# Performance work log

Measured on AMD Instinct MI355X. Metric: run time of the kernel, lower is better.

Reference implementation:

```python
import jax, jax.numpy as jnp
import numpy as np

N, B, D, S, STDDEV = 129, 128, 64, 2, 0.5  # N odd so the site before the last is an input site
NOUT = int(np.ceil((N - 1) / S) + 1)  # 65
NIN = N - NOUT                        # 64


def setup_inputs() -> dict:
    key = jax.random.key(0)
    k1, k2, k3 = jax.random.split(key, 3)
    x = jax.random.normal(k1, (N, B, 2), jnp.float32)
    mps_input = STDDEV * jax.random.normal(k2, (NIN, D, D, 2), jnp.float32)
    mps_output = STDDEV * jax.random.normal(k3, (NOUT, D, D, 2, 2), jnp.float32)
    return {"x": x, "mps_input": mps_input, "mps_output": mps_output}


def _forward(x, mps_input, mps_output):
    # ---- batched MPS contraction (call) ----
    # S=2: even sites are output sites, odd sites are input sites.
    X = jnp.einsum('nbi,nlrij->nblrj', x[::2], mps_output)      # (Nout,B,D,D,2)
    A_in = jnp.einsum('nbi,nlri->nblr', x[1::2], mps_input)     # (Nin,B,D,D)
    # middle mps blocks: A_in[k-1] contracted with X[k] for k=1..Nout-2
    mps_mid = jnp.einsum('nblr,nbrdi->nbldi', A_in[:-1], X[1:-1])   # (Nout-2,B,D,D,2)
    mps_last = jnp.einsum('blr,brdi->bldi', A_in[-1], X[-1][:, :, :1])  # (B,D,1,2)
    A0 = X[0][:, 0]  # first block restricted to l=0 -> (B,D,2)

    Al = jnp.einsum('bui,bdi->bud', A0, A0)  # (B,D,D), PSD

    def step(Al, A):
        amax = jnp.max(jnp.abs(Al), axis=(1, 2), keepdims=True)
        Aln = Al / amax
        T = jnp.einsum('bdu,bdli->blui', Aln, A)
        return jnp.einsum('blui,buri->blr', T, A), jnp.log(amax[:, 0, 0])

    Al, logs = jax.lax.scan(step, Al, mps_mid)   # logs: (Nout-2, B)
    Al, last_log = step(Al, mps_last)            # Al: (B,1,1)
    out = jnp.sum(logs, axis=0) + last_log + jnp.log(Al[:, 0, 0])  # (B,)

    # ---- log_norm: scalar DxD transfer-matrix chain ----
    Al0 = jnp.zeros((D, D), x.dtype).at[0, 0].set(1.0)

    def contract_out(M2, Mo):
        T = jnp.einsum('du,dkij->kuij', M2, Mo)
        return jnp.einsum('kuij,ulij->kl', T, Mo)

    def contract_in(M2, Mi):
        T = jnp.einsum('du,dki->kui', M2, Mi)
        return jnp.einsum('kui,uli->kl', T, Mi)

    # site 0: amax of initial Al is exactly 1 (log 0), then contract output tensor 0
    Aln = contract_out(Al0, mps_output[0])

    def nstep(M2, Ms):
        Mi, Mo = Ms
        a1 = jnp.max(jnp.abs(M2)); M2 = contract_in(M2 / a1, Mi)
        a2 = jnp.max(jnp.abs(M2)); M2 = contract_out(M2 / a2, Mo)
        return M2, jnp.log(a1) + jnp.log(a2)

    AlN, nlogs = jax.lax.scan(nstep, Aln, (mps_input, mps_output[1:]))
    lnrm = jnp.sum(nlogs) + jnp.log(AlN[0, 0])
    return out, lnrm


def reference(x, mps_input, mps_output):
    return _forward(x, mps_input, mps_output)
```

## Files before the change

### kernel.cpp

```cpp
#include <hip/hip_runtime.h>
#include <math.h>

#define TPB 512
#define LDM 72
#define SLOTS 4608


typedef __attribute__((ext_vector_type(8))) short bf16x8;
typedef __attribute__((ext_vector_type(4))) float f32x4;
typedef unsigned short US;

__device__ __forceinline__ US f2b(float f) {
    union { float f; unsigned u; } v; v.f = f;
    return (US)((v.u + 0x7FFFu + ((v.u >> 16) & 1u)) >> 16);
}
__device__ __forceinline__ float bf2f(US h) {
    union { unsigned u; float f; } v; v.u = ((unsigned)h) << 16; return v.f;
}

struct Frag { bf16x8 lo, hi; };

__device__ __forceinline__ Frag ldf(const US* buf, int row0, int lane) {
    const US* p = buf + (row0 + (lane & 15)) * LDM + ((lane >> 4) << 3);
    Frag f; f.lo = *(const bf16x8*)p; f.hi = *(const bf16x8*)(p + 32); return f;
}
__device__ __forceinline__ f32x4 mm(const Frag& a, const Frag& b, f32x4 c) {
    c = __builtin_amdgcn_mfma_f32_16x16x32_bf16(a.lo, b.lo, c, 0, 0, 0);
    c = __builtin_amdgcn_mfma_f32_16x16x32_bf16(a.hi, b.hi, c, 0, 0, 0);
    return c;
}
__device__ __forceinline__ void stt(US* dst, f32x4 d, float s,
                                    int col0, int row0, int lane) {
    ushort4 wv;
    wv.x = f2b(d.x * s); wv.y = f2b(d.y * s);
    wv.z = f2b(d.z * s); wv.w = f2b(d.w * s);
    *(ushort4*)(dst + (col0 + (lane & 15)) * LDM + row0 + ((lane >> 4) << 2)) = wv;
}

template<int NG>
__device__ __forceinline__ void congr16(US* sm, int sSlot, int gSlot, US* Uw,
                                        f32x4 acc[4], int C0, int lane) {
    const US* S = sm + sSlot * SLOTS;
    Frag aS[4];
#pragma unroll
    for (int rt = 0; rt < 4; ++rt) aS[rt] = ldf(S, rt * 16, lane);
#pragma unroll
    for (int g = 0; g < NG; ++g) {
        const US* G = sm + (gSlot + g) * SLOTS;
        US* Ug = Uw + g * (16 * LDM);
        Frag b = ldf(G, C0, lane);
#pragma unroll
        for (int rt = 0; rt < 4; ++rt) {
            f32x4 z = {0.f, 0.f, 0.f, 0.f};
            z = mm(aS[rt], b, z);
            stt(Ug, z, 1.f, 0, rt * 16, lane);
        }
    }
#pragma unroll
    for (int rt = 0; rt < 4; ++rt) acc[rt] = (f32x4){0.f, 0.f, 0.f, 0.f};
#pragma unroll
    for (int g = 0; g < NG; ++g) {
        const US* G = sm + (gSlot + g) * SLOTS;
        const US* Ug = Uw + g * (16 * LDM);
        Frag u = ldf(Ug, 0, lane);
#pragma unroll
        for (int rt = 0; rt < 4; ++rt) {
            Frag ga = ldf(G, rt * 16, lane);
            acc[rt] = mm(ga, u, acc[rt]);
        }
    }
}

__device__ __forceinline__ void stacc16(US* Sb, const f32x4 acc[4], float s,
                                        int C0, int lane) {
#pragma unroll
    for (int rt = 0; rt < 4; ++rt) stt(Sb, acc[rt], s, C0, rt * 16, lane);
}

__device__ __forceinline__ float stmax16(US* Sb, const f32x4 acc[4], float s,
                                         int C0, int lane) {
    float m = 0.f;
#pragma unroll
    for (int rt = 0; rt < 4; ++rt) {
        float vx = acc[rt].x * s, vy = acc[rt].y * s;
        float vz = acc[rt].z * s, vw = acc[rt].w * s;
        m = fmaxf(m, fmaxf(fmaxf(fabsf(vx), fabsf(vy)),
                           fmaxf(fabsf(vz), fabsf(vw))));
        ushort4 wv; wv.x = f2b(vx); wv.y = f2b(vy); wv.z = f2b(vz); wv.w = f2b(vw);
        *(ushort4*)(Sb + (C0 + (lane & 15)) * LDM + rt * 16 + ((lane >> 4) << 2)) = wv;
    }
#pragma unroll
    for (int off = 32; off; off >>= 1) m = fmaxf(m, __shfl_down(m, off, 64));
    return m;
}

__global__ __launch_bounds__(TPB)
void mps_proj_kernel(const float* __restrict__ x,
                     const float* __restrict__ mi,
                     const float* __restrict__ mo,
                     float* __restrict__ out) {
    __shared__ __align__(16) US smem[12 * SLOTS];
#define SL(i) (smem + (i) * SLOTS)
    __shared__ float fsA[256];
    __shared__ float fsp[8];
    __shared__ float fsrA[2][4];
    __shared__ float fsrB[2][4];
    __shared__ float fsv[128];

    const int tid  = threadIdx.x;
    const int lane = tid & 63;
    const int w    = tid >> 6;
    const int C0   = (w & 3) * 16;
    US* const Uw   = smem + (8 + (w & 3)) * SLOTS;

    const float2* mi2 = (const float2*)mi;
    const float4* mo4 = (const float4*)mo;

    float logsum = 0.f;
    f32x4 acc[4];

    if (blockIdx.x < 128) {
        const int b = blockIdx.x;
        const float xa = x[b * 2 + 0], xb = x[b * 2 + 1];
        if (tid < 64) {
            float4 v = mo4[tid];
            fsA[tid * 2 + 0] = xa * v.x + xb * v.z;
            fsA[tid * 2 + 1] = xa * v.y + xb * v.w;
        }
        __syncthreads();
        float vals[8]; float mloc = 0.f;
#pragma unroll
        for (int j = 0; j < 8; ++j) {
            int pos = tid + j * TPB; int u = pos >> 6, d = pos & 63;
            float s = fsA[u * 2] * fsA[d * 2] + fsA[u * 2 + 1] * fsA[d * 2 + 1];
            vals[j] = s; mloc = fmaxf(mloc, fabsf(s));
        }
#pragma unroll
        for (int off = 32; off; off >>= 1) mloc = fmaxf(mloc, __shfl_down(mloc, off, 64));
        if (lane == 0) fsp[w] = mloc;
        __syncthreads();
        float amax = fsp[0];
#pragma unroll
        for (int i = 1; i < 8; ++i) amax = fmaxf(amax, fsp[i]);
        logsum = logf(amax);
        {
            float inv = 1.f / amax;
#pragma unroll
            for (int j = 0; j < 8; ++j) {
                int pos = tid + j * TPB;
                SL(0)[(pos >> 6) * LDM + (pos & 63)] = f2b(vals[j] * inv);
            }
        }
        if (w >= 4) {
            const int j = w - 4;
            const float x1a = x[256 + b * 2 + 0], x1b = x[256 + b * 2 + 1];
            bf16x8 g0, g1;
#pragma unroll
            for (int t = 0; t < 8; ++t) {
                float2 m0 = mi2[(16 * j + t) * 64 + lane];
                float2 m1 = mi2[(16 * j + 8 + t) * 64 + lane];
                g0[t] = (short)f2b(x1a * m0.x + x1b * m0.y);
                g1[t] = (short)f2b(x1a * m1.x + x1b * m1.y);
            }
            *(bf16x8*)(SL(2) + lane * LDM + 16 * j) = g0;
            *(bf16x8*)(SL(2) + lane * LDM + 16 * j + 8) = g1;
        }
        if (tid < 4) fsrB[1][tid] = 1.f;
        __syncthreads();

        for (int k = 0; k < 63; ++k) {
            if (w < 4) {
                congr16<1>(smem, 0, 2, Uw, acc, C0, lane);
                stacc16(SL(1), acc, 1.f, C0, lane);
            } else {
                const int j = w - 4;
                const float x0a = x[(2 * k + 2) * 256 + b * 2 + 0];
                const float x0b = x[(2 * k + 2) * 256 + b * 2 + 1];
                const float4* so = mo4 + (k + 1) * 4096;
                bf16x8 a0, a1, c0, c1;
#pragma unroll
                for (int t = 0; t < 8; ++t) {
                    float4 m0 = so[(16 * j + t) * 64 + lane];
                    float4 m1 = so[(16 * j + 8 + t) * 64 + lane];
                    a0[t] = (short)f2b(x0a * m0.x + x0b * m0.z);
                    c0[t] = (short)f2b(x0a * m0.y + x0b * m0.w);
                    a1[t] = (short)f2b(x0a * m1.x + x0b * m1.z);
                    c1[t] = (short)f2b(x0a * m1.y + x0b * m1.w);
                }
                *(bf16x8*)(SL(4) + lane * LDM + 16 * j) = a0;
                *(bf16x8*)(SL(4) + lane * LDM + 16 * j + 8) = a1;
                *(bf16x8*)(SL(5) + lane * LDM + 16 * j) = c0;
                *(bf16x8*)(SL(5) + lane * LDM + 16 * j + 8) = c1;
            }
            __syncthreads();
            if (w < 4) {
                float a = fmaxf(fmaxf(fsrB[(k + 1) & 1][0], fsrB[(k + 1) & 1][1]),
                                fmaxf(fsrB[(k + 1) & 1][2], fsrB[(k + 1) & 1][3]));
                logsum += logf(a);
                congr16<2>(smem, 1, 4, Uw, acc, C0, lane);
                float m = stmax16(SL(0), acc, 1.f / a, C0, lane);
                if (lane == 0) fsrB[k & 1][w] = m;
            } else {
                const int j = w - 4;
                const float x1a = x[(2 * k + 3) * 256 + b * 2 + 0];
                const float x1b = x[(2 * k + 3) * 256 + b * 2 + 1];
                const float2* si = mi2 + (k + 1) * 4096;
                bf16x8 g0, g1;
#pragma unroll
                for (int t = 0; t < 8; ++t) {
                    float2 m0 = si[(16 * j + t) * 64 + lane];
                    float2 m1 = si[(16 * j + 8 + t) * 64 + lane];
                    g0[t] = (short)f2b(x1a * m0.x + x1b * m0.y);
                    g1[t] = (short)f2b(x1a * m1.x + x1b * m1.y);
                }
                *(bf16x8*)(SL(2) + lane * LDM + 16 * j) = g0;
                *(bf16x8*)(SL(2) + lane * LDM + 16 * j + 8) = g1;
            }
            __syncthreads();
        }

        {
            const float x0a = x[128 * 256 + b * 2 + 0];
            const float x0b = x[128 * 256 + b * 2 + 1];
            if (tid < 64) {
                float4 v = mo4[64 * 4096 + tid * 64];
                fsA[tid * 2 + 0] = x0a * v.x + x0b * v.z;
                fsA[tid * 2 + 1] = x0a * v.y + x0b * v.w;
            }
            __syncthreads();
            if (tid < 128) {
                int dd = tid >> 1, ii = tid & 1;
                float s = 0.f;
                for (int r = 0; r < 64; ++r)
                    s += bf2f(SL(2)[r * LDM + dd]) * fsA[r * 2 + ii];
                fsv[tid] = s;
            }
            __syncthreads();
            float part = 0.f;
#pragma unroll
            for (int j = 0; j < 8; ++j) {
                int pos = tid + j * TPB; int dd = pos >> 6, uu = pos & 63;
                part += bf2f(SL(0)[dd * LDM + uu]) *
                        (fsv[dd * 2] * fsv[uu * 2] + fsv[dd * 2 + 1] * fsv[uu * 2 + 1]);
            }
#pragma unroll
            for (int off = 32; off; off >>= 1) part += __shfl_down(part, off, 64);
            if (lane == 0) fsp[w] = part;
            __syncthreads();
            if (tid == 0) {
                float t = 0.f;
#pragma unroll
                for (int i = 0; i < 8; ++i) t += fsp[i];
                out[b] = logsum + logf(t);
            }
        }
    } else {
        if (tid < 64) {
            float4 v = mo4[tid];
            fsA[tid * 4 + 0] = v.x; fsA[tid * 4 + 1] = v.y;
            fsA[tid * 4 + 2] = v.z; fsA[tid * 4 + 3] = v.w;
        }
        __syncthreads();
        float vals[8]; float mloc = 0.f;
#pragma unroll
        for (int j = 0; j < 8; ++j) {
            int pos = tid + j * TPB; int kk = pos >> 6, ll = pos & 63;
            float s = fsA[kk*4+0]*fsA[ll*4+0] + fsA[kk*4+1]*fsA[ll*4+1] +
                      fsA[kk*4+2]*fsA[ll*4+2] + fsA[kk*4+3]*fsA[ll*4+3];
            vals[j] = s; mloc = fmaxf(mloc, fabsf(s));
        }
#pragma unroll
        for (int off = 32; off; off >>= 1) mloc = fmaxf(mloc, __shfl_down(mloc, off, 64));
        if (lane == 0) fsp[w] = mloc;
        __syncthreads();
        float amax = fsp[0];
#pragma unroll
        for (int i = 1; i < 8; ++i) amax = fmaxf(amax, fsp[i]);
        logsum = logf(amax);
        {
            float inv = 1.f / amax;
#pragma unroll
            for (int j = 0; j < 8; ++j) {
                int pos = tid + j * TPB;
                SL(0)[(pos >> 6) * LDM + (pos & 63)] = f2b(vals[j] * inv);
            }
        }
        if (w >= 4) {
            const int j = w - 4;
            bf16x8 g00, g01, g10, g11;
#pragma unroll
            for (int t = 0; t < 8; ++t) {
                float2 m0 = mi2[(16 * j + t) * 64 + lane];
                float2 m1 = mi2[(16 * j + 8 + t) * 64 + lane];
                g00[t] = (short)f2b(m0.x); g10[t] = (short)f2b(m0.y);
                g01[t] = (short)f2b(m1.x); g11[t] = (short)f2b(m1.y);
            }
            *(bf16x8*)(SL(2) + lane * LDM + 16 * j) = g00;
            *(bf16x8*)(SL(2) + lane * LDM + 16 * j + 8) = g01;
            *(bf16x8*)(SL(3) + lane * LDM + 16 * j) = g10;
            *(bf16x8*)(SL(3) + lane * LDM + 16 * j + 8) = g11;
        }
        if (tid < 4) fsrB[1][tid] = 1.f;
        __syncthreads();

        for (int n = 0; n < 64; ++n) {
            if (w < 4) {
                float aB = fmaxf(fmaxf(fsrB[(n + 1) & 1][0], fsrB[(n + 1) & 1][1]),
                                 fmaxf(fsrB[(n + 1) & 1][2], fsrB[(n + 1) & 1][3]));
                logsum += logf(aB);
                congr16<2>(smem, 0, 2, Uw, acc, C0, lane);
                float m = stmax16(SL(1), acc, 1.f / aB, C0, lane);
                if (lane == 0) fsrA[n & 1][w] = m;
            } else {
                const int j = w - 4;
                const float4* so = mo4 + (n + 1) * 4096;
                bf16x8 g[4][2];
#pragma unroll
                for (int t = 0; t < 8; ++t) {
                    float4 m0 = so[(16 * j + t) * 64 + lane];
                    float4 m1 = so[(16 * j + 8 + t) * 64 + lane];
                    g[0][0][t] = (short)f2b(m0.x); g[1][0][t] = (short)f2b(m0.y);
                    g[2][0][t] = (short)f2b(m0.z); g[3][0][t] = (short)f2b(m0.w);
                    g[0][1][t] = (short)f2b(m1.x); g[1][1][t] = (short)f2b(m1.y);
                    g[2][1][t] = (short)f2b(m1.z); g[3][1][t] = (short)f2b(m1.w);
                }
#pragma unroll
                for (int c = 0; c < 4; ++c) {
                    *(bf16x8*)(SL(4 + c) + lane * LDM + 16 * j) = g[c][0];
                    *(bf16x8*)(SL(4 + c) + lane * LDM + 16 * j + 8) = g[c][1];
                }
            }
            __syncthreads();
            if (w < 4) {
                float aA = fmaxf(fmaxf(fsrA[n & 1][0], fsrA[n & 1][1]),
                                 fmaxf(fsrA[n & 1][2], fsrA[n & 1][3]));
                logsum += logf(aA);
                congr16<4>(smem, 1, 4, Uw, acc, C0, lane);
                float m = stmax16(SL(0), acc, 1.f / aA, C0, lane);
                if (lane == 0) fsrB[n & 1][w] = m;
            } else if (n < 63) {
                const int j = w - 4;
                const float2* si = mi2 + (n + 1) * 4096;
                bf16x8 g00, g01, g10, g11;
#pragma unroll
                for (int t = 0; t < 8; ++t) {
                    float2 m0 = si[(16 * j + t) * 64 + lane];
                    float2 m1 = si[(16 * j + 8 + t) * 64 + lane];
                    g00[t] = (short)f2b(m0.x); g10[t] = (short)f2b(m0.y);
                    g01[t] = (short)f2b(m1.x); g11[t] = (short)f2b(m1.y);
                }
                *(bf16x8*)(SL(2) + lane * LDM + 16 * j) = g00;
                *(bf16x8*)(SL(2) + lane * LDM + 16 * j + 8) = g01;
                *(bf16x8*)(SL(3) + lane * LDM + 16 * j) = g10;
                *(bf16x8*)(SL(3) + lane * LDM + 16 * j + 8) = g11;
            }
            __syncthreads();
        }
        if (tid == 0) out[128] = logsum + logf(bf2f(SL(0)[0]));
    }
#undef SL
}

extern "C" void kernel_launch(void* const* d_in, const int* in_sizes, int n_in,
                              void* d_out, int out_size, void* d_ws, size_t ws_size,
                              hipStream_t stream) {
    (void)in_sizes; (void)n_in; (void)d_ws; (void)ws_size; (void)out_size;
    const float* x  = (const float*)d_in[0];
    const float* mi = (const float*)d_in[1];
    const float* mo = (const float*)d_in[2];
    float* out = (float*)d_out;
    hipLaunchKernelGGL(mps_proj_kernel, dim3(129), dim3(TPB), 0, stream,
                       x, mi, mo, out);
}
```

Measured before the change: 262.6 us.

## Compute full 64x64 congruence in one wave with double-buffered loader waves

The chain contraction moves from four compute waves, each owning a 16-column strip and syncing twice per step with shared-memory amax exchange, to a single wave that computes the whole 64x64 product per half-step and computes the amax in registers. Four loader waves (block shrinks to 320 threads) prefetch both input and output tensors for the next step into double-buffered LDS slots, so there is only one barrier per step. This removes cross-wave reductions and half the barriers, at the cost of serializing four times the MFMA work onto one wave per block.

```diff
diff --git a/kernel.cpp b/kernel.cpp
--- a/kernel.cpp
+++ b/kernel.cpp
@@ -1,7 +1,7 @@
 #include <hip/hip_runtime.h>
 #include <math.h>
 
-#define TPB 512
+#define TPB 320
 #define LDM 72
 #define SLOTS 4608
 
@@ -38,60 +38,62 @@
 }
 
 template<int NG>
-__device__ __forceinline__ void congr16(US* sm, int sSlot, int gSlot, US* Uw,
-                                        f32x4 acc[4], int C0, int lane) {
-    const US* S = sm + sSlot * SLOTS;
+__device__ __forceinline__ void congr_full(US* sm, const US* S, const US* Gb,
+                                           f32x4 acc[4][4], int lane) {
     Frag aS[4];
 #pragma unroll
     for (int rt = 0; rt < 4; ++rt) aS[rt] = ldf(S, rt * 16, lane);
 #pragma unroll
+    for (int rt = 0; rt < 4; ++rt)
+#pragma unroll
+        for (int ct = 0; ct < 4; ++ct) acc[rt][ct] = (f32x4){0.f, 0.f, 0.f, 0.f};
+#pragma unroll
     for (int g = 0; g < NG; ++g) {
-        const US* G = sm + (gSlot + g) * SLOTS;
-        US* Ug = Uw + g * (16 * LDM);
-        Frag b = ldf(G, C0, lane);
-#pragma unroll
-        for (int rt = 0; rt < 4; ++rt) {
-            f32x4 z = {0.f, 0.f, 0.f, 0.f};
-            z = mm(aS[rt], b, z);
-            stt(Ug, z, 1.f, 0, rt * 16, lane);
+        const US* G = Gb + g * SLOTS;
+        US* U = sm + (1 + 13 * (g & 1)) * SLOTS;
+#pragma unroll
+        for (int ct = 0; ct < 4; ++ct) {
+            Frag bG = ldf(G, ct * 16, lane);
+#pragma unroll
+            for (int rt = 0; rt < 4; ++rt) {
+                f32x4 d = {0.f, 0.f, 0.f, 0.f};
+                d = mm(aS[rt], bG, d);
+                stt(U, d, 1.f, ct * 16, rt * 16, lane);
+            }
+        }
+        Frag gA[4];
+#pragma unroll
+        for (int rt = 0; rt < 4; ++rt) gA[rt] = ldf(G, rt * 16, lane);
+#pragma unroll
+        for (int ct = 0; ct < 4; ++ct) {
+            Frag bU = ldf(U, ct * 16, lane);
+#pragma unroll
+            for (int rt = 0; rt < 4; ++rt)
+                acc[rt][ct] = mm(gA[rt], bU, acc[rt][ct]);
         }
     }
-#pragma unroll
-    for (int rt = 0; rt < 4; ++rt) acc[rt] = (f32x4){0.f, 0.f, 0.f, 0.f};
-#pragma unroll
-    for (int g = 0; g < NG; ++g) {
-        const US* G = sm + (gSlot + g) * SLOTS;
-        const US* Ug = Uw + g * (16 * LDM);
-        Frag u = ldf(Ug, 0, lane);
-#pragma unroll
-        for (int rt = 0; rt < 4; ++rt) {
-            Frag ga = ldf(G, rt * 16, lane);
-            acc[rt] = mm(ga, u, acc[rt]);
-        }
-    }
-}
-
-__device__ __forceinline__ void stacc16(US* Sb, const f32x4 acc[4], float s,
-                                        int C0, int lane) {
-#pragma unroll
-    for (int rt = 0; rt < 4; ++rt) stt(Sb, acc[rt], s, C0, rt * 16, lane);
-}
-
-__device__ __forceinline__ float stmax16(US* Sb, const f32x4 acc[4], float s,
-                                         int C0, int lane) {
+}
+
+__device__ __forceinline__ float amax16(const f32x4 acc[4][4]) {
     float m = 0.f;
 #pragma unroll
-    for (int rt = 0; rt < 4; ++rt) {
-        float vx = acc[rt].x * s, vy = acc[rt].y * s;
-        float vz = acc[rt].z * s, vw = acc[rt].w * s;
-        m = fmaxf(m, fmaxf(fmaxf(fabsf(vx), fabsf(vy)),
-                           fmaxf(fabsf(vz), fabsf(vw))));
-        ushort4 wv; wv.x = f2b(vx); wv.y = f2b(vy); wv.z = f2b(vz); wv.w = f2b(vw);
-        *(ushort4*)(Sb + (C0 + (lane & 15)) * LDM + rt * 16 + ((lane >> 4) << 2)) = wv;
-    }
-#pragma unroll
-    for (int off = 32; off; off >>= 1) m = fmaxf(m, __shfl_down(m, off, 64));
+    for (int rt = 0; rt < 4; ++rt)
+#pragma unroll
+        for (int ct = 0; ct < 4; ++ct)
+            m = fmaxf(m, fmaxf(fmaxf(fabsf(acc[rt][ct].x), fabsf(acc[rt][ct].y)),
+                               fmaxf(fabsf(acc[rt][ct].z), fabsf(acc[rt][ct].w))));
+#pragma unroll
+    for (int off = 32; off; off >>= 1) m = fmaxf(m, __shfl_xor(m, off, 64));
     return m;
+}
+
+__device__ __forceinline__ void store16(US* dst, const f32x4 acc[4][4], float s,
+                                        int lane) {
+#pragma unroll
+    for (int rt = 0; rt < 4; ++rt)
+#pragma unroll
+        for (int ct = 0; ct < 4; ++ct)
+            stt(dst, acc[rt][ct], s, ct * 16, rt * 16, lane);
 }
 
 __global__ __launch_bounds__(TPB)
@@ -99,25 +101,21 @@
                      const float* __restrict__ mi,
                      const float* __restrict__ mo,
                      float* __restrict__ out) {
-    __shared__ __align__(16) US smem[12 * SLOTS];
+    __shared__ __align__(16) US smem[15 * SLOTS];
 #define SL(i) (smem + (i) * SLOTS)
     __shared__ float fsA[256];
-    __shared__ float fsp[8];
-    __shared__ float fsrA[2][4];
-    __shared__ float fsrB[2][4];
+    __shared__ float fsr[8];
     __shared__ float fsv[128];
 
     const int tid  = threadIdx.x;
     const int lane = tid & 63;
     const int w    = tid >> 6;
-    const int C0   = (w & 3) * 16;
-    US* const Uw   = smem + (8 + (w & 3)) * SLOTS;
 
     const float2* mi2 = (const float2*)mi;
     const float4* mo4 = (const float4*)mo;
 
     float logsum = 0.f;
-    f32x4 acc[4];
+    f32x4 acc[4][4];
 
     if (blockIdx.x < 128) {
         const int b = blockIdx.x;
@@ -128,93 +126,109 @@
             fsA[tid * 2 + 1] = xa * v.y + xb * v.w;
         }
         __syncthreads();
-        float vals[8]; float mloc = 0.f;
-#pragma unroll
-        for (int j = 0; j < 8; ++j) {
-            int pos = tid + j * TPB; int u = pos >> 6, d = pos & 63;
+        float mloc = 0.f;
+        for (int pos = tid; pos < 4096; pos += TPB) {
+            int u = pos >> 6, d = pos & 63;
             float s = fsA[u * 2] * fsA[d * 2] + fsA[u * 2 + 1] * fsA[d * 2 + 1];
-            vals[j] = s; mloc = fmaxf(mloc, fabsf(s));
+            mloc = fmaxf(mloc, fabsf(s));
         }
 #pragma unroll
         for (int off = 32; off; off >>= 1) mloc = fmaxf(mloc, __shfl_down(mloc, off, 64));
-        if (lane == 0) fsp[w] = mloc;
-        __syncthreads();
-        float amax = fsp[0];
-#pragma unroll
-        for (int i = 1; i < 8; ++i) amax = fmaxf(amax, fsp[i]);
+        if (lane == 0) fsr[w] = mloc;
+        __syncthreads();
+        float amax = fsr[0];
+#pragma unroll
+        for (int i = 1; i < 5; ++i) amax = fmaxf(amax, fsr[i]);
         logsum = logf(amax);
         {
             float inv = 1.f / amax;
-#pragma unroll
-            for (int j = 0; j < 8; ++j) {
-                int pos = tid + j * TPB;
-                SL(0)[(pos >> 6) * LDM + (pos & 63)] = f2b(vals[j] * inv);
-            }
-        }
-        if (w >= 4) {
-            const int j = w - 4;
+            for (int pos = tid; pos < 4096; pos += TPB) {
+                int u = pos >> 6, d = pos & 63;
+                float s = fsA[u * 2] * fsA[d * 2] + fsA[u * 2 + 1] * fsA[d * 2 + 1];
+                SL(0)[u * LDM + d] = f2b(s * inv);
+            }
+        }
+        if (w >= 1) {
+            const int j = w - 1;
             const float x1a = x[256 + b * 2 + 0], x1b = x[256 + b * 2 + 1];
-            bf16x8 g0, g1;
+            const float x0a = x[512 + b * 2 + 0], x0b = x[512 + b * 2 + 1];
+            const float4* so = mo4 + 4096;
+            bf16x8 g0, g1, a0, a1, c0, c1;
 #pragma unroll
             for (int t = 0; t < 8; ++t) {
                 float2 m0 = mi2[(16 * j + t) * 64 + lane];
                 float2 m1 = mi2[(16 * j + 8 + t) * 64 + lane];
                 g0[t] = (short)f2b(x1a * m0.x + x1b * m0.y);
                 g1[t] = (short)f2b(x1a * m1.x + x1b * m1.y);
+                float4 o0 = so[(16 * j + t) * 64 + lane];
+                float4 o1 = so[(16 * j + 8 + t) * 64 + lane];
+                a0[t] = (short)f2b(x0a * o0.x + x0b * o0.z);
+                c0[t] = (short)f2b(x0a * o0.y + x0b * o0.w);
+                a1[t] = (short)f2b(x0a * o1.x + x0b * o1.z);
+                c1[t] = (short)f2b(x0a * o1.y + x0b * o1.w);
             }
             *(bf16x8*)(SL(2) + lane * LDM + 16 * j) = g0;
             *(bf16x8*)(SL(2) + lane * LDM + 16 * j + 8) = g1;
-        }
-        if (tid < 4) fsrB[1][tid] = 1.f;
+            *(bf16x8*)(SL(6) + lane * LDM + 16 * j) = a0;
+            *(bf16x8*)(SL(6) + lane * LDM + 16 * j + 8) = a1;
+            *(bf16x8*)(SL(7) + lane * LDM + 16 * j) = c0;
+            *(bf16x8*)(SL(7) + lane * LDM + 16 * j + 8) = c1;
+        }
         __syncthreads();
 
         for (int k = 0; k < 63; ++k) {
-            if (w < 4) {
-                congr16<1>(smem, 0, 2, Uw, acc, C0, lane);
-                stacc16(SL(1), acc, 1.f, C0, lane);
+            const int p = k & 1, np = 1 - p;
+            if (w == 0) {
+                congr_full<1>(smem, SL(0), SL(2 + p * 2), acc, lane);
+                store16(SL(0), acc, 1.f, lane);
+                congr_full<2>(smem, SL(0), SL(6 + p * 4), acc, lane);
+                float m = amax16(acc);
+                logsum += logf(m);
+                store16(SL(0), acc, 1.f / m, lane);
             } else {
-                const int j = w - 4;
-                const float x0a = x[(2 * k + 2) * 256 + b * 2 + 0];
-                const float x0b = x[(2 * k + 2) * 256 + b * 2 + 1];
-                const float4* so = mo4 + (k + 1) * 4096;
-                bf16x8 a0, a1, c0, c1;
-#pragma unroll
-                for (int t = 0; t < 8; ++t) {
-                    float4 m0 = so[(16 * j + t) * 64 + lane];
-                    float4 m1 = so[(16 * j + 8 + t) * 64 + lane];
-                    a0[t] = (short)f2b(x0a * m0.x + x0b * m0.z);
-                    c0[t] = (short)f2b(x0a * m0.y + x0b * m0.w);
-                    a1[t] = (short)f2b(x0a * m1.x + x0b * m1.z);
-                    c1[t] = (short)f2b(x0a * m1.y + x0b * m1.w);
+                const int j = w - 1;
+                if (k < 62) {
+                    const float x1a = x[(2 * k + 3) * 256 + b * 2 + 0];
+                    const float x1b = x[(2 * k + 3) * 256 + b * 2 + 1];
+                    const float x0a = x[(2 * k + 4) * 256 + b * 2 + 0];
+                    const float x0b = x[(2 * k + 4) * 256 + b * 2 + 1];
+                    const float2* si = mi2 + (k + 1) * 4096;
+                    const float4* so = mo4 + (k + 2) * 4096;
+                    bf16x8 g0, g1, a0, a1, c0, c1;
+#pragma unroll
+                    for (int t = 0; t < 8; ++t) {
+                        float2 m0 = si[(16 * j + t) * 64 + lane];
+                        float2 m1 = si[(16 * j + 8 + t) * 64 + lane];
+                        g0[t] = (short)f2b(x1a * m0.x + x1b * m0.y);
+                        g1[t] = (short)f2b(x1a * m1.x + x1b * m1.y);
+                        float4 o0 = so[(16 * j + t) * 64 + lane];
+                        float4 o1 = so[(16 * j + 8 + t) * 64 + lane];
+                        a0[t] = (short)f2b(x0a * o0.x + x0b * o0.z);
+                        c0[t] = (short)f2b(x0a * o0.y + x0b * o0.w);
+                        a1[t] = (short)f2b(x0a * o1.x + x0b * o1.z);
+                        c1[t] = (short)f2b(x0a * o1.y + x0b * o1.w);
+                    }
+                    *(bf16x8*)(SL(2 + np * 2) + lane * LDM + 16 * j) = g0;
+                    *(bf16x8*)(SL(2 + np * 2) + lane * LDM + 16 * j + 8) = g1;
+                    *(bf16x8*)(SL(6 + np * 4) + lane * LDM + 16 * j) = a0;
+                    *(bf16x8*)(SL(6 + np * 4) + lane * LDM + 16 * j + 8) = a1;
+                    *(bf16x8*)(SL(7 + np * 4) + lane * LDM + 16 * j) = c0;
+                    *(bf16x8*)(SL(7 + np * 4) + lane * LDM + 16 * j + 8) = c1;
+                } else {
+                    const float x1a = x[127 * 256 + b * 2 + 0];
+                    const float x1b = x[127 * 256 + b * 2 + 1];
+                    const float2* si = mi2 + 63 * 4096;
+                    bf16x8 g0, g1;
+#pragma unroll
+                    for (int t = 0; t < 8; ++t) {
+                        float2 m0 = si[(16 * j + t) * 64 + lane];
+                        float2 m1 = si[(16 * j + 8 + t) * 64 + lane];
+                        g0[t] = (short)f2b(x1a * m0.x + x1b * m0.y);
+                        g1[t] = (short)f2b(x1a * m1.x + x1b * m1.y);
+                    }
+                    *(bf16x8*)(SL(4) + lane * LDM + 16 * j) = g0;
+                    *(bf16x8*)(SL(4) + lane * LDM + 16 * j + 8) = g1;
                 }
-                *(bf16x8*)(SL(4) + lane * LDM + 16 * j) = a0;
-                *(bf16x8*)(SL(4) + lane * LDM + 16 * j + 8) = a1;
-                *(bf16x8*)(SL(5) + lane * LDM + 16 * j) = c0;
-                *(bf16x8*)(SL(5) + lane * LDM + 16 * j + 8) = c1;
-            }
-            __syncthreads();
-            if (w < 4) {
-                float a = fmaxf(fmaxf(fsrB[(k + 1) & 1][0], fsrB[(k + 1) & 1][1]),
-                                fmaxf(fsrB[(k + 1) & 1][2], fsrB[(k + 1) & 1][3]));
-                logsum += logf(a);
-                congr16<2>(smem, 1, 4, Uw, acc, C0, lane);
-                float m = stmax16(SL(0), acc, 1.f / a, C0, lane);
-                if (lane == 0) fsrB[k & 1][w] = m;
-            } else {
-                const int j = w - 4;
-                const float x1a = x[(2 * k + 3) * 256 + b * 2 + 0];
-                const float x1b = x[(2 * k + 3) * 256 + b * 2 + 1];
-                const float2* si = mi2 + (k + 1) * 4096;
-                bf16x8 g0, g1;
-#pragma unroll
-                for (int t = 0; t < 8; ++t) {
-                    float2 m0 = si[(16 * j + t) * 64 + lane];
-                    float2 m1 = si[(16 * j + 8 + t) * 64 + lane];
-                    g0[t] = (short)f2b(x1a * m0.x + x1b * m0.y);
-                    g1[t] = (short)f2b(x1a * m1.x + x1b * m1.y);
-                }
-                *(bf16x8*)(SL(2) + lane * LDM + 16 * j) = g0;
-                *(bf16x8*)(SL(2) + lane * LDM + 16 * j + 8) = g1;
             }
             __syncthreads();
         }
@@ -232,25 +246,24 @@
                 int dd = tid >> 1, ii = tid & 1;
                 float s = 0.f;
                 for (int r = 0; r < 64; ++r)
-                    s += bf2f(SL(2)[r * LDM + dd]) * fsA[r * 2 + ii];
+                    s += bf2f(SL(4)[r * LDM + dd]) * fsA[r * 2 + ii];
                 fsv[tid] = s;
             }
             __syncthreads();
             float part = 0.f;
-#pragma unroll
-            for (int j = 0; j < 8; ++j) {
-                int pos = tid + j * TPB; int dd = pos >> 6, uu = pos & 63;
+            for (int pos = tid; pos < 4096; pos += TPB) {
+                int dd = pos >> 6, uu = pos & 63;
                 part += bf2f(SL(0)[dd * LDM + uu]) *
                         (fsv[dd * 2] * fsv[uu * 2] + fsv[dd * 2 + 1] * fsv[uu * 2 + 1]);
             }
 #pragma unroll
             for (int off = 32; off; off >>= 1) part += __shfl_down(part, off, 64);
-            if (lane == 0) fsp[w] = part;
+            if (lane == 0) fsr[w] = part;
             __syncthreads();
             if (tid == 0) {
                 float t = 0.f;
 #pragma unroll
-                for (int i = 0; i < 8; ++i) t += fsp[i];
+                for (int i = 0; i < 5; ++i) t += fsr[i];
                 out[b] = logsum + logf(t);
             }
         }
@@ -261,102 +274,106 @@
             fsA[tid * 4 + 2] = v.z; fsA[tid * 4 + 3] = v.w;
         }
         __syncthreads();
-        float vals[8]; float mloc = 0.f;
-#pragma unroll
-        for (int j = 0; j < 8; ++j) {
-            int pos = tid + j * TPB; int kk = pos >> 6, ll = pos & 63;
+        float mloc = 0.f;
+        for (int pos = tid; pos < 4096; pos += TPB) {
+            int kk = pos >> 6, ll = pos & 63;
             float s = fsA[kk*4+0]*fsA[ll*4+0] + fsA[kk*4+1]*fsA[ll*4+1] +
                       fsA[kk*4+2]*fsA[ll*4+2] + fsA[kk*4+3]*fsA[ll*4+3];
-            vals[j] = s; mloc = fmaxf(mloc, fabsf(s));
+            mloc = fmaxf(mloc, fabsf(s));
         }
 #pragma unroll
         for (int off = 32; off; off >>= 1) mloc = fmaxf(mloc, __shfl_down(mloc, off, 64));
-        if (lane == 0) fsp[w] = mloc;
-        __syncthreads();
-        float amax = fsp[0];
-#pragma unroll
-        for (int i = 1; i < 8; ++i) amax = fmaxf(amax, fsp[i]);
+        if (lane == 0) fsr[w] = mloc;
+        __syncthreads();
+        float amax = fsr[0];
+#pragma unroll
+        for (int i = 1; i < 5; ++i) amax = fmaxf(amax, fsr[i]);
         logsum = logf(amax);
         {
             float inv = 1.f / amax;
-#pragma unroll
-            for (int j = 0; j < 8; ++j) {
-                int pos = tid + j * TPB;
-                SL(0)[(pos >> 6) * LDM + (pos & 63)] = f2b(vals[j] * inv);
-            }
-        }
-        if (w >= 4) {
-            const int j = w - 4;
+            for (int pos = tid; pos < 4096; pos += TPB) {
+                int kk = pos >> 6, ll = pos & 63;
+                float s = fsA[kk*4+0]*fsA[ll*4+0] + fsA[kk*4+1]*fsA[ll*4+1] +
+                          fsA[kk*4+2]*fsA[ll*4+2] + fsA[kk*4+3]*fsA[ll*4+3];
+                SL(0)[kk * LDM + ll] = f2b(s * inv);
+            }
+        }
+        if (w >= 1) {
+            const int j = w - 1;
+            const float4* so = mo4 + 4096;
             bf16x8 g00, g01, g10, g11;
+            bf16x8 o[4][2];
 #pragma unroll
             for (int t = 0; t < 8; ++t) {
                 float2 m0 = mi2[(16 * j + t) * 64 + lane];
                 float2 m1 = mi2[(16 * j + 8 + t) * 64 + lane];
                 g00[t] = (short)f2b(m0.x); g10[t] = (short)f2b(m0.y);
                 g01[t] = (short)f2b(m1.x); g11[t] = (short)f2b(m1.y);
+                float4 o0 = so[(16 * j + t) * 64 + lane];
+                float4 o1 = so[(16 * j + 8 + t) * 64 + lane];
+                o[0][0][t] = (short)f2b(o0.x); o[1][0][t] = (short)f2b(o0.y);
+                o[2][0][t] = (short)f2b(o0.z); o[3][0][t] = (short)f2b(o0.w);
+                o[0][1][t] = (short)f2b(o1.x); o[1][1][t] = (short)f2b(o1.y);
+                o[2][1][t] = (short)f2b(o1.z); o[3][1][t] = (short)f2b(o1.w);
             }
             *(bf16x8*)(SL(2) + lane * LDM + 16 * j) = g00;
             *(bf16x8*)(SL(2) + lane * LDM + 16 * j + 8) = g01;
             *(bf16x8*)(SL(3) + lane * LDM + 16 * j) = g10;
             *(bf16x8*)(SL(3) + lane * LDM + 16 * j + 8) = g11;
-        }
-        if (tid < 4) fsrB[1][tid] = 1.f;
+#pragma unroll
+            for (int c = 0; c < 4; ++c) {
+                *(bf16x8*)(SL(6 + c) + lane * LDM + 16 * j) = o[c][0];
+                *(bf16x8*)(SL(6 + c) + lane * LDM + 16 * j + 8) = o[c][1];
+            }
+        }
         __syncthreads();
 
         for (int n = 0; n < 64; ++n) {
-            if (w < 4) {
-                float aB = fmaxf(fmaxf(fsrB[(n + 1) & 1][0], fsrB[(n + 1) & 1][1]),
-                                 fmaxf(fsrB[(n + 1) & 1][2], fsrB[(n + 1) & 1][3]));
-                logsum += logf(aB);
-                congr16<2>(smem, 0, 2, Uw, acc, C0, lane);
-                float m = stmax16(SL(1), acc, 1.f / aB, C0, lane);
-                if (lane == 0) fsrA[n & 1][w] = m;
-            } else {
-                const int j = w - 4;
-                const float4* so = mo4 + (n + 1) * 4096;
-                bf16x8 g[4][2];
-#pragma unroll
-                for (int t = 0; t < 8; ++t) {
-                    float4 m0 = so[(16 * j + t) * 64 + lane];
-                    float4 m1 = so[(16 * j + 8 + t) * 64 + lane];
-                    g[0][0][t] = (short)f2b(m0.x); g[1][0][t] = (short)f2b(m0.y);
-                    g[2][0][t] = (short)f2b(m0.z); g[3][0][t] = (short)f2b(m0.w);
-                    g[0][1][t] = (short)f2b(m1.x); g[1][1][t] = (short)f2b(m1.y);
-                    g[2][1][t] = (short)f2b(m1.z); g[3][1][t] = (short)f2b(m1.w);
+            const int p = n & 1, np = 1 - p;
+            if (w == 0) {
+                congr_full<2>(smem, SL(0), SL(2 + p * 2), acc, lane);
+                float a2 = amax16(acc);
+                logsum += logf(a2);
+                store16(SL(0), acc, 1.f / a2, lane);
+                congr_full<4>(smem, SL(0), SL(6 + p * 4), acc, lane);
+                if (n < 63) {
+                    float a1 = amax16(acc);
+                    logsum += logf(a1);
+                    store16(SL(0), acc, 1.f / a1, lane);
+                } else {
+                    if (lane == 0) out[128] = logsum + logf(acc[0][0].x);
                 }
-#pragma unroll
-                for (int c = 0; c < 4; ++c) {
-                    *(bf16x8*)(SL(4 + c) + lane * LDM + 16 * j) = g[c][0];
-                    *(bf16x8*)(SL(4 + c) + lane * LDM + 16 * j + 8) = g[c][1];
-                }
-            }
-            __syncthreads();
-            if (w < 4) {
-                float aA = fmaxf(fmaxf(fsrA[n & 1][0], fsrA[n & 1][1]),
-                                 fmaxf(fsrA[n & 1][2], fsrA[n & 1][3]));
-                logsum += logf(aA);
-                congr16<4>(smem, 1, 4, Uw, acc, C0, lane);
-                float m = stmax16(SL(0), acc, 1.f / aA, C0, lane);
-                if (lane == 0) fsrB[n & 1][w] = m;
             } else if (n < 63) {
-                const int j = w - 4;
+                const int j = w - 1;
                 const float2* si = mi2 + (n + 1) * 4096;
+                const float4* so = mo4 + (n + 2) * 4096;
                 bf16x8 g00, g01, g10, g11;
+                bf16x8 o[4][2];
 #pragma unroll
                 for (int t = 0; t < 8; ++t) {
                     float2 m0 = si[(16 * j + t) * 64 + lane];
                     float2 m1 = si[(16 * j + 8 + t) * 64 + lane];
                     g00[t] = (short)f2b(m0.x); g10[t] = (short)f2b(m0.y);
                     g01[t] = (short)f2b(m1.x); g11[t] = (short)f2b(m1.y);
+                    float4 o0 = so[(16 * j + t) * 64 + lane];
+                    float4 o1 = so[(16 * j + 8 + t) * 64 + lane];
+                    o[0][0][t] = (short)f2b(o0.x); o[1][0][t] = (short)f2b(o0.y);
+                    o[2][0][t] = (short)f2b(o0.z); o[3][0][t] = (short)f2b(o0.w);
+                    o[0][1][t] = (short)f2b(o1.x); o[1][1][t] = (short)f2b(o1.y);
+                    o[2][1][t] = (short)f2b(o1.z); o[3][1][t] = (short)f2b(o1.w);
                 }
-                *(bf16x8*)(SL(2) + lane * LDM + 16 * j) = g00;
-                *(bf16x8*)(SL(2) + lane * LDM + 16 * j + 8) = g01;
-                *(bf16x8*)(SL(3) + lane * LDM + 16 * j) = g10;
-                *(bf16x8*)(SL(3) + lane * LDM + 16 * j + 8) = g11;
-            }
-            __syncthreads();
-        }
-        if (tid == 0) out[128] = logsum + logf(bf2f(SL(0)[0]));
+                *(bf16x8*)(SL(2 + np * 2) + lane * LDM + 16 * j) = g00;
+                *(bf16x8*)(SL(2 + np * 2) + lane * LDM + 16 * j + 8) = g01;
+                *(bf16x8*)(SL(3 + np * 2) + lane * LDM + 16 * j) = g10;
+                *(bf16x8*)(SL(3 + np * 2) + lane * LDM + 16 * j + 8) = g11;
+#pragma unroll
+                for (int c = 0; c < 4; ++c) {
+                    *(bf16x8*)(SL(6 + np * 4 + c) + lane * LDM + 16 * j) = o[c][0];
+                    *(bf16x8*)(SL(6 + np * 4 + c) + lane * LDM + 16 * j + 8) = o[c][1];
+                }
+            }
+            __syncthreads();
+        }
     }
 #undef SL
 }
```

Measured after the change: 598.4 us. +127.9%, slower.
